# Kernel tuning notes

Measured on AMD Instinct MI355X. Metric: run time of the kernel, lower is better.

The kernel has to match this reference:

```python
import jax, jax.numpy as jnp
import numpy as np

N_QUBITS = 8
DEPTH = 1
INPUT_DIM = 64
HIDDEN = 8  # must equal N_QUBITS
SEQ = 64
BATCH = 256


def _apply_rx(state, wire, ang):
    # state: (B, 2, 2, ..., 2) with wire w on axis 1+w; ang: (B,) angles
    n = state.ndim - 1
    st = jnp.moveaxis(state, 1 + wire, -1)
    a0, a1 = st[..., 0], st[..., 1]
    half = ang * 0.5
    c = jnp.cos(half).reshape((-1,) + (1,) * (n - 1))
    s = jnp.sin(half).reshape((-1,) + (1,) * (n - 1))
    new = jnp.stack([c * a0 - 1j * s * a1, c * a1 - 1j * s * a0], axis=-1)
    return jnp.moveaxis(new, -1, 1 + wire)


def _apply_cnot(state, cw, tw):
    st = jnp.moveaxis(state, (1 + cw, 1 + tw), (-2, -1))
    st = st.at[..., 1, :].set(st[..., 1, ::-1])  # flip target where control=1
    return jnp.moveaxis(st, (-2, -1), (1 + cw, 1 + tw))


def qgate(theta, qparams):
    # theta: (B, n) data-dependent RX angles; qparams: (n,) trainable RX angles
    B, n = theta.shape
    state = jnp.zeros((B,) + (2,) * n, dtype=jnp.complex64)
    state = state.at[(slice(None),) + (0,) * n].set(1.0 + 0.0j)  # |0...0>
    for w in range(n):
        state = _apply_rx(state, w, theta[:, w])
    for w in range(n - 1):
        state = _apply_cnot(state, w, w + 1)
    for w in range(n):
        state = _apply_rx(state, w, jnp.broadcast_to(qparams[w], (B,)))
    probs = jnp.abs(state) ** 2  # (B, 2, ..., 2)
    expz = []
    for w in range(n):
        pw = probs.sum(axis=tuple(a for a in range(1, n + 1) if a != 1 + w))  # (B, 2)
        expz.append(pw[:, 0] - pw[:, 1])  # <Z_w>
    return jnp.stack(expz, axis=1)  # (B, n)


def setup_inputs() -> dict:
    key = jax.random.key(0)
    ks = jax.random.split(key, 13)
    d_in = INPUT_DIM + HIDDEN
    d_out = N_QUBITS * DEPTH
    sc = 1.0 / np.sqrt(d_in)
    inp = {"inputs": jax.random.normal(ks[0], (SEQ, BATCH, INPUT_DIM), dtype=jnp.float32)}
    names = ["f", "i", "g", "o"]
    for j, nm in enumerate(names):
        inp["W" + nm] = jax.random.uniform(ks[1 + 3 * j], (d_out, d_in), minval=-sc, maxval=sc, dtype=jnp.float32)
        inp["b" + nm] = jax.random.uniform(ks[2 + 3 * j], (d_out,), minval=-sc, maxval=sc, dtype=jnp.float32)
        inp["q" + nm] = jax.random.normal(ks[3 + 3 * j], (d_out,), dtype=jnp.float32)
    return inp


def reference(inputs, Wf, bf, qf, Wi, bi, qi, Wg, bg, qg, Wo, bo, qo):
    B = inputs.shape[1]
    hx0 = jnp.zeros((B, HIDDEN), dtype=inputs.dtype)
    cx0 = jnp.zeros((B, HIDDEN), dtype=inputs.dtype)

    def step(carry, x_t):
        hx, cx = carry
        comb = jnp.concatenate([x_t, hx], axis=1)  # (B, input+hidden)
        f = jax.nn.sigmoid(qgate(comb @ Wf.T + bf, qf))
        i_ = jax.nn.sigmoid(qgate(comb @ Wi.T + bi, qi))
        g = jnp.tanh(qgate(comb @ Wg.T + bg, qg))
        o = jax.nn.sigmoid(qgate(comb @ Wo.T + bo, qo))
        cx = f * cx + i_ * g
        hx = o * jnp.tanh(cx)
        return (hx, cx), hx

    (hx, cx), outputs = jax.lax.scan(step, (hx0, cx0), inputs)
    return outputs, (hx, cx)
```

## Files before the change

### kernel.cpp

```cpp
#include <hip/hip_runtime.h>
#include <hip/hip_bf16.h>

__device__ float g_pre_static[8 * 1024 * 1024];

__device__ __forceinline__ float rcp_(float x)   { return __builtin_amdgcn_rcpf(x); }
__device__ __forceinline__ float sigm_f(float x) { return rcp_(1.0f + __expf(-x)); }
__device__ __forceinline__ float tanh_f(float x) { return 1.0f - 2.0f*rcp_(__expf(2.0f*x) + 1.0f); }
__device__ __forceinline__ float sigm(float x)  { return 1.0f/(1.0f + __expf(-x)); }
__device__ __forceinline__ float tanh_(float x) { float e = __expf(2.0f*x); return (e-1.0f)/(e+1.0f); }

template<int CTRL>
__device__ __forceinline__ float dppf(float x) {
    return __int_as_float(__builtin_amdgcn_update_dpp(
        0, __float_as_int(x), CTRL, 0xF, 0xF, true));
}

template<int IDD>
__global__ __launch_bounds__(64) void k_pre8(
    const float* __restrict__ x_,
    const float* __restrict__ W0, const float* __restrict__ b0p,
    const float* __restrict__ W1, const float* __restrict__ b1p,
    const float* __restrict__ W2, const float* __restrict__ b2p,
    const float* __restrict__ W3, const float* __restrict__ b3p,
    float* __restrict__ pre, int S, int B)
{
    constexpr int DIN = IDD + 8;
    __shared__ float wsh[32 * IDD];
    __shared__ float sb32[32];
    const int t   = blockIdx.x;
    const int tid = threadIdx.x;
    const long b  = (long)blockIdx.y * 64 + tid;
    const float* Wp[4] = {W0, W1, W2, W3};
    const float* bp[4] = {b0p, b1p, b2p, b3p};

    #pragma unroll
    for (int it = 0; it < (32*IDD)/64; ++it) {
        int idx = it*64 + tid;
        int gw = idx / IDD, k = idx % IDD;
        wsh[idx] = Wp[gw >> 3][(gw & 7)*DIN + k];
    }
    if (tid < 32) sb32[tid] = bp[tid >> 3][tid & 7];
    __syncthreads();

    if (b >= B) return;
    float xr[IDD];
    const float4* xv = (const float4*)(x_ + ((long)t*B + b)*IDD);
    #pragma unroll
    for (int i = 0; i < IDD/4; ++i) {
        float4 v = xv[i];
        xr[4*i] = v.x; xr[4*i+1] = v.y; xr[4*i+2] = v.z; xr[4*i+3] = v.w;
    }

    float acc[32];
    #pragma unroll
    for (int gw = 0; gw < 32; ++gw) {
        float a = sb32[gw];
        const float4* wr = (const float4*)&wsh[gw*IDD];
        #pragma unroll
        for (int k4 = 0; k4 < IDD/4; ++k4) {
            float4 wv = wr[k4];
            a += xr[4*k4]*wv.x + xr[4*k4+1]*wv.y + xr[4*k4+2]*wv.z + xr[4*k4+3]*wv.w;
        }
        acc[gw] = a;
    }
    float4* op = (float4*)(pre + ((long)t*B + b)*32);
    #pragma unroll
    for (int i = 0; i < 8; ++i) {
        #define SRC(o) (((((o) >> 4)*2 + ((o) & 1))*8) + ((((o) & 15)) >> 1))
        op[i] = make_float4(acc[SRC(4*i)], acc[SRC(4*i+1)],
                            acc[SRC(4*i+2)], acc[SRC(4*i+3)]);
        #undef SRC
    }
}

__global__ __launch_bounds__(256) void k_pre_gen(
    const float* __restrict__ x_,
    const float* W0, const float* b0p,
    const float* W1, const float* b1p,
    const float* W2, const float* b2p,
    const float* W3, const float* b3p,
    float* __restrict__ pre,
    int S, int B, int ID, int H, int SP)
{
    extern __shared__ float lds[];
    const int dIn  = ID + H;
    const int dInP = dIn + 1;
    float* xs    = lds;
    float* wsh   = lds + 64*SP;
    float* sbias = wsh + 4*H*dInP;
    const int t   = blockIdx.x;
    const int tid = threadIdx.x;
    const int bl  = tid & 63;
    const int q   = tid >> 6;
    const int b0  = blockIdx.y * 64;
    const float* Wp[4] = {W0, W1, W2, W3};
    const float* bp[4] = {b0p, b1p, b2p, b3p};

    for (int g = 0; g < 4; ++g)
        for (int idx = tid; idx < H*dIn; idx += 256) {
            int w = idx / dIn, k = idx - w*dIn;
            wsh[(g*H + w)*dInP + k] = Wp[g][idx];
        }
    for (int idx = tid; idx < 4*H; idx += 256)
        sbias[idx] = bp[idx / H][idx % H];

    {
        int total = 64 * ID;
        for (int i = tid; i < total; i += 256) {
            int r = i / ID, c = i - r*ID;
            long bb = (long)b0 + r; if (bb >= B) bb = B - 1;
            xs[r*SP + c] = x_[((long)t*B + bb)*ID + c];
        }
    }
    __syncthreads();

    const int b = b0 + bl;
    if (b < B) {
        const float* xrow = &xs[bl*SP];
        float* orow = pre + (((long)t*B + b)*4 + q)*H;
        for (int w = 0; w < H; ++w) {
            float acc = sbias[q*H + w];
            const float* wrow = &wsh[(q*H + w)*dInP];
            for (int k = 0; k < ID; ++k) acc += xrow[k] * wrow[k];
            orow[w] = acc;
        }
    }
}

__global__ __launch_bounds__(64) void k_rec8(
    const float* __restrict__ W0, const float* __restrict__ q0,
    const float* __restrict__ W1, const float* __restrict__ q1,
    const float* __restrict__ W2, const float* __restrict__ q2,
    const float* __restrict__ W3, const float* __restrict__ q3,
    const float* __restrict__ pre,
    float* __restrict__ out, int S, int B, int ID)
{
    const int dIn  = ID + 8;
    const int lane = threadIdx.x;
    const int w    = lane & 7;
    const int gp   = (lane >> 3) & 1;
    const int b    = blockIdx.x*4 + (lane >> 4);
    const int bs   = (b < B) ? b : (B - 1);
    const float* Wp[4] = {W0, W1, W2, W3};
    const float* qp[4] = {q0, q1, q2, q3};
    const int g0 = 2*gp, g1 = 2*gp + 1;

    float wrot0[8], wrot1[8];
    #pragma unroll
    for (int k = 0; k < 8; ++k) {
        int j = (w - k) & 7;
        wrot0[k] = Wp[g0][(long)w*dIn + ID + j];
        wrot1[k] = Wp[g1][(long)w*dIn + ID + j];
    }
    const float qv0 = qp[g0][w], qv1 = qp[g1][w];
    const float mult0 = (w < 7) ? __cosf(qv0) : 1.0f;
    const float mult1 = (w < 7) ? __cosf(qv1) : 1.0f;
    const float qadd0 = (w == 7) ? qv0 : 0.0f;
    const float qadd1 = (w == 7) ? qv1 : 0.0f;
    const float ascl = gp ? 2.0f : 1.0f;
    const float aoff = gp ? -1.0f : 0.0f;

    float cxw = 0.0f, hxw = 0.0f;
    float hxr[8];
    #pragma unroll
    for (int k = 0; k < 8; ++k) hxr[k] = 0.0f;

    const float2* base = (const float2*)(pre + (long)bs*32 + gp*16 + 2*w);
    const long tstep = (long)B*16;

    float2 pf[4];
    #pragma unroll
    for (int d = 0; d < 4; ++d) {
        int tt = (d < S) ? d : (S - 1);
        pf[d] = base[(long)tt*tstep];
    }

    for (int t0 = 0; t0 < S; t0 += 4) {
        #pragma unroll
        for (int d = 0; d < 4; ++d) {
            const int t = t0 + d;
            if (t < S) {
                float2 pc = pf[d];
                int tn = t + 4; if (tn >= S) tn = S - 1;
                pf[d] = base[(long)tn*tstep];

                float th0 = pc.x, th1 = pc.y;
                #pragma unroll
                for (int k = 0; k < 8; ++k) {
                    th0 = fmaf(wrot0[k], hxr[k], th0);
                    th1 = fmaf(wrot1[k], hxr[k], th1);
                }
                float P0 = __cosf(th0 + qadd0);
                float P1 = __cosf(th1 + qadd1);

                float s;
                s = dppf<0x111>(P0); P0 *= (w >= 1) ? s : 1.0f;
                s = dppf<0x111>(P1); P1 *= (w >= 1) ? s : 1.0f;
                s = dppf<0x112>(P0); P0 *= (w >= 2) ? s : 1.0f;
                s = dppf<0x112>(P1); P1 *= (w >= 2) ? s : 1.0f;
                s = dppf<0x114>(P0); P0 *= (w >= 4) ? s : 1.0f;
                s = dppf<0x114>(P1); P1 *= (w >= 4) ? s : 1.0f;

                float act0 = ascl * sigm_f(ascl * (mult0 * P0)) + aoff;
                float act1 = sigm_f(mult1 * P1);

                float ex0 = dppf<0x128>(act0);
                float ex1 = dppf<0x128>(act1);
                float fv = gp ? ex0  : act0;
                float iv = gp ? ex1  : act1;
                float gv = gp ? act0 : ex0;
                float ov = gp ? act1 : ex1;

                cxw = fv*cxw + iv*gv;
                hxw = ov * tanh_f(cxw);

                if (gp == 0 && b < B) out[((long)t*B + b)*8 + w] = hxw;

                hxr[0] = hxw;
                hxr[1] = dppf<0x121>(hxw);
                hxr[2] = dppf<0x122>(hxw);
                hxr[3] = dppf<0x123>(hxw);
                hxr[4] = dppf<0x124>(hxw);
                hxr[5] = dppf<0x125>(hxw);
                hxr[6] = dppf<0x126>(hxw);
                hxr[7] = dppf<0x127>(hxw);
            }
        }
    }

    if (gp == 0 && b < B) {
        out[((long)S*B + b)*8 + w]     = hxw;
        out[((long)S*B + B + b)*8 + w] = cxw;
    }
}

__global__ __launch_bounds__(64) void k_rec_g(
    const float* __restrict__ pre,
    const float* W0, const float* q0,
    const float* W1, const float* q1,
    const float* W2, const float* q2,
    const float* W3, const float* q3,
    float* __restrict__ out, int S, int B, int ID, int H)
{
    __shared__ float sWh[4*32*32];
    __shared__ float scq[4*32];
    const int dIn = ID + H;
    const int tid = threadIdx.x;
    const int b   = blockIdx.x*64 + tid;
    const float* Wp[4] = {W0, W1, W2, W3};
    const float* qp[4] = {q0, q1, q2, q3};

    for (int idx = tid; idx < 4*H*H; idx += 64) {
        int g = idx / (H*H), r = idx % (H*H);
        int w = r / H, j = r % H;
        sWh[(g*H + w)*H + j] = Wp[g][(long)w*dIn + ID + j];
    }
    for (int idx = tid; idx < 4*H; idx += 64) {
        int g = idx / H, w = idx % H;
        float qv = qp[g][w];
        scq[idx] = (w < H-1) ? __cosf(qv) : qv;
    }
    __syncthreads();
    if (b >= B) return;

    float hx[32], cx[32], gate[4][32], th[32];
    for (int w = 0; w < H; ++w) { hx[w] = 0.0f; cx[w] = 0.0f; }

    for (int t = 0; t < S; ++t) {
        const float* pt = pre + ((long)t*B + b)*4*H;
        for (int g = 0; g < 4; ++g) {
            for (int w = 0; w < H; ++w) {
                float a = pt[g*H + w];
                const float* wrp = &sWh[(g*H + w)*H];
                for (int j = 0; j < H; ++j) a += wrp[j]*hx[j];
                th[w] = a;
            }
            float cum = 1.0f;
            for (int w = 0; w < H-1; ++w) {
                cum *= __cosf(th[w]);
                gate[g][w] = scq[g*H + w] * cum;
            }
            gate[g][H-1] = cum * __cosf(th[H-1] + scq[g*H + H-1]);
        }
        float* orow = out + ((long)t*B + b)*H;
        for (int w = 0; w < H; ++w) {
            float fv = sigm (gate[0][w]);
            float iv = sigm (gate[1][w]);
            float gv = tanh_(gate[2][w]);
            float ov = sigm (gate[3][w]);
            cx[w] = fv*cx[w] + iv*gv;
            hx[w] = ov*tanh_(cx[w]);
            orow[w] = hx[w];
        }
    }
    float* oh = out + ((long)S*B + b)*H;
    float* oc = out + ((long)S*B + B + b)*H;
    for (int w = 0; w < H; ++w) { oh[w] = hx[w]; oc[w] = cx[w]; }
}

static bool derive(long sz[13], long osz, long& S, long& B, long& ID, long& H) {
    H = sz[3];
    long dIn = (H > 0) ? sz[1] / H : 0;
    ID = dIn - H;
    long TB = (ID > 0) ? sz[0] / ID : 0;
    B = (H > 0) ? (osz / H - TB) / 2 : 0;
    S = (B > 0) ? TB / B : 0;
    return (H >= 1 && H <= 32 && ID >= 1 && B >= 1 && S >= 1 &&
            S*B == TB && (S*B + 2*B)*H == osz &&
            dIn*H == sz[1] && TB*ID == sz[0]);
}

extern "C" void kernel_launch(void* const* d_in, const int* in_sizes, int n_in,
                              void* d_out, int out_size, void* d_ws, size_t ws_size,
                              hipStream_t stream) {
    const float* x  = (const float*)d_in[0];
    const float* Wf = (const float*)d_in[1];  const float* bfv = (const float*)d_in[2];  const float* qf = (const float*)d_in[3];
    const float* Wi = (const float*)d_in[4];  const float* biv = (const float*)d_in[5];  const float* qi = (const float*)d_in[6];
    const float* Wg = (const float*)d_in[7];  const float* bgv = (const float*)d_in[8];  const float* qg = (const float*)d_in[9];
    const float* Wo = (const float*)d_in[10]; const float* bov = (const float*)d_in[11]; const float* qo = (const float*)d_in[12];
    float* out = (float*)d_out;

    long S = 0, B = 0, ID = 0, H = 0;
    bool ok = false;
    for (int scale : {1, 4, 2}) {
        long sz[13];
        for (int i = 0; i < 13; ++i) sz[i] = (long)in_sizes[i] / scale;
        long osz = (long)out_size / scale;
        if (derive(sz, osz, S, B, ID, H)) { ok = true; break; }
    }
    if (!ok) { H = 8; ID = 64; B = 256; S = 64; }
    long dIn = ID + H;

    size_t pre_bytes = (size_t)S * 4 * H * B * sizeof(float);
    float* pre = (ws_size >= pre_bytes) ? (float*)d_ws : g_pre_static;

    if (H == 8 && ID == 64) {
        k_pre8<64><<<dim3((unsigned)S, (unsigned)((B + 63) / 64)), dim3(64), 0, stream>>>(
            x, Wf, bfv, Wi, biv, Wg, bgv, Wo, bov, pre, (int)S, (int)B);
        k_rec8<<<dim3((unsigned)((B + 3) / 4)), dim3(64), 0, stream>>>(
            Wf, qf, Wi, qi, Wg, qg, Wo, qo, pre, out, (int)S, (int)B, (int)ID);
    } else {
        int SP = (int)ID + 1;
        size_t lds_bytes = (size_t)(64*SP + 4*H*(dIn + 1) + 4*H) * sizeof(float);
        k_pre_gen<<<dim3((unsigned)S, (unsigned)((B + 63) / 64)), dim3(256), lds_bytes, stream>>>(
            x, Wf, bfv, Wi, biv, Wg, bgv, Wo, bov, pre,
            (int)S, (int)B, (int)ID, (int)H, SP);
        k_rec_g<<<dim3((unsigned)((B + 63) / 64)), dim3(64), 0, stream>>>(
            pre, Wf, qf, Wi, qi, Wg, qg, Wo, qo, out, (int)S, (int)B, (int)ID, (int)H);
    }
}
```

Before: 111.8 us.

## Parallelize input projection over output units with per-thread weight rows

```diff
diff --git a/kernel.cpp b/kernel.cpp
--- a/kernel.cpp
+++ b/kernel.cpp
@@ -16,7 +16,7 @@
 }
 
 template<int IDD>
-__global__ __launch_bounds__(64) void k_pre8(
+__global__ __launch_bounds__(256) void k_pre8(
     const float* __restrict__ x_,
     const float* __restrict__ W0, const float* __restrict__ b0p,
     const float* __restrict__ W1, const float* __restrict__ b1p,
@@ -25,52 +25,45 @@
     float* __restrict__ pre, int S, int B)
 {
     constexpr int DIN = IDD + 8;
-    __shared__ float wsh[32 * IDD];
-    __shared__ float sb32[32];
+    __shared__ float xs[8][IDD];
     const int t   = blockIdx.x;
     const int tid = threadIdx.x;
-    const long b  = (long)blockIdx.y * 64 + tid;
+    const int bl  = tid >> 5;
+    const int l   = tid & 31;
+    const int gp  = l >> 4, w = (l >> 1) & 7, e = l & 1;
+    const int g   = 2*gp + e;
+    const long b0 = (long)blockIdx.y * 8;
     const float* Wp[4] = {W0, W1, W2, W3};
     const float* bp[4] = {b0p, b1p, b2p, b3p};
 
-    #pragma unroll
-    for (int it = 0; it < (32*IDD)/64; ++it) {
-        int idx = it*64 + tid;
-        int gw = idx / IDD, k = idx % IDD;
-        wsh[idx] = Wp[gw >> 3][(gw & 7)*DIN + k];
-    }
-    if (tid < 32) sb32[tid] = bp[tid >> 3][tid & 7];
-    __syncthreads();
-
-    if (b >= B) return;
-    float xr[IDD];
-    const float4* xv = (const float4*)(x_ + ((long)t*B + b)*IDD);
-    #pragma unroll
-    for (int i = 0; i < IDD/4; ++i) {
-        float4 v = xv[i];
-        xr[4*i] = v.x; xr[4*i+1] = v.y; xr[4*i+2] = v.z; xr[4*i+3] = v.w;
-    }
-
-    float acc[32];
-    #pragma unroll
-    for (int gw = 0; gw < 32; ++gw) {
-        float a = sb32[gw];
-        const float4* wr = (const float4*)&wsh[gw*IDD];
+    if (tid < 8*(IDD/4)) {
+        int r = tid / (IDD/4), k4 = tid % (IDD/4);
+        long bb = b0 + r; if (bb >= B) bb = B - 1;
+        float4 v = ((const float4*)(x_ + ((long)t*B + bb)*IDD))[k4];
+        ((float4*)&xs[r][0])[k4] = v;
+    }
+
+    float wr[IDD];
+    {
+        const float4* wv = (const float4*)(Wp[g] + (long)w*DIN);
         #pragma unroll
         for (int k4 = 0; k4 < IDD/4; ++k4) {
-            float4 wv = wr[k4];
-            a += xr[4*k4]*wv.x + xr[4*k4+1]*wv.y + xr[4*k4+2]*wv.z + xr[4*k4+3]*wv.w;
-        }
-        acc[gw] = a;
-    }
-    float4* op = (float4*)(pre + ((long)t*B + b)*32);
+            float4 v = wv[k4];
+            wr[4*k4] = v.x; wr[4*k4+1] = v.y; wr[4*k4+2] = v.z; wr[4*k4+3] = v.w;
+        }
+    }
+    float a = bp[g][w];
+    __syncthreads();
+
+    const long b = b0 + bl;
+    if (b >= B) return;
+    const float4* xv = (const float4*)&xs[bl][0];
     #pragma unroll
-    for (int i = 0; i < 8; ++i) {
-        #define SRC(o) (((((o) >> 4)*2 + ((o) & 1))*8) + ((((o) & 15)) >> 1))
-        op[i] = make_float4(acc[SRC(4*i)], acc[SRC(4*i+1)],
-                            acc[SRC(4*i+2)], acc[SRC(4*i+3)]);
-        #undef SRC
-    }
+    for (int k4 = 0; k4 < IDD/4; ++k4) {
+        float4 v = xv[k4];
+        a += wr[4*k4]*v.x + wr[4*k4+1]*v.y + wr[4*k4+2]*v.z + wr[4*k4+3]*v.w;
+    }
+    pre[((long)t*B + b)*32 + l] = a;
 }
 
 __global__ __launch_bounds__(256) void k_pre_gen(
@@ -335,7 +328,7 @@
     float* pre = (ws_size >= pre_bytes) ? (float*)d_ws : g_pre_static;
 
     if (H == 8 && ID == 64) {
-        k_pre8<64><<<dim3((unsigned)S, (unsigned)((B + 63) / 64)), dim3(64), 0, stream>>>(
+        k_pre8<64><<<dim3((unsigned)S, (unsigned)((B + 7) / 8)), dim3(256), 0, stream>>>(
             x, Wf, bfv, Wi, biv, Wg, bgv, Wo, bov, pre, (int)S, (int)B);
         k_rec8<<<dim3((unsigned)((B + 3) / 4)), dim3(64), 0, stream>>>(
             Wf, qf, Wi, qi, Wg, qg, Wo, qo, pre, out, (int)S, (int)B, (int)ID);
```

Measured after the change: 102.8 us. 1.09x faster.
